# Kernel tuning notes

Hardware: AMD Instinct MI355X
Metric: run time of the kernel (lower is better)

The kernel has to match this reference:

```python
import jax, jax.numpy as jnp
import numpy as np

HEADS = 16
DIM_HEAD = 64
HEIGHT = 16
KERNEL = 5
DILATION = 1
ALPHA = 32 ** 2


def stable_softmax(t, axis=-1, alpha=ALPHA):
    t = t / alpha
    t = t - jax.lax.stop_gradient(jnp.max(t, axis=axis, keepdims=True))
    return jax.nn.softmax(t * alpha, axis=axis)


def setup_inputs() -> dict:
    key = jax.random.key(0)
    ks = jax.random.split(key, 5)
    b, n, dim = 4, 4097, 1024
    inner = HEADS * DIM_HEAD
    x = jax.random.normal(ks[0], (b, n, dim), dtype=jnp.float32)
    w_qkv = jax.random.normal(ks[1], (dim, 3 * inner), dtype=jnp.float32) * (dim ** -0.5)
    w_out = jax.random.normal(ks[2], (inner, dim), dtype=jnp.float32) * (inner ** -0.5)
    b_out = jax.random.normal(ks[3], (dim,), dtype=jnp.float32) * 0.02
    w_th = jax.random.normal(ks[4], (HEADS, HEADS), dtype=jnp.float32) * (HEADS ** -0.5)
    return {"x": x, "w_qkv": w_qkv, "w_out": w_out, "b_out": b_out, "w_th": w_th}


def reference(x, w_qkv, w_out, b_out, w_th):
    b, n, dim = x.shape
    h, d = HEADS, DIM_HEAD
    height, K, dil = HEIGHT, KERNEL, DILATION
    pad = dil * (K - 1) // 2
    scale = d ** -0.5
    kernel_numel = K * height

    # pad (n-1) non-BOS tokens to a multiple of height (static shapes)
    seq_pad = (-(n - 1)) % height
    xp = jnp.pad(x, ((0, 0), (0, seq_pad), (0, 0))) if seq_pad > 0 else x

    qkv = xp @ w_qkv  # [b, np, 3*inner]
    q, k, v = jnp.split(qkv, 3, axis=-1)

    if n == 1:  # bos-only path
        return v @ w_out + b_out

    out_bos = v[:, :1]  # [b, 1, inner]

    def to_heads(t):
        return t.reshape(b, -1, h, d).transpose(0, 2, 1, 3)  # [b,h,np,d]

    q, k, v = map(to_heads, (q, k, v))
    q = q * scale

    k_bos, k = k[:, :, 0], k[:, :, 1:]
    v_bos, v = v[:, :, 0], v[:, :, 1:]
    q = q[:, :, 1:]

    X = q.shape[2] // height  # number of timesteps

    # k, v as 2D grids [b,h,X,height,d]; unfold local windows along timestep axis
    k = k.reshape(b, h, X, height, d)
    v = v.reshape(b, h, X, height, d)
    kp = jnp.pad(k, ((0, 0), (0, 0), (pad, pad), (0, 0), (0, 0)))
    vp = jnp.pad(v, ((0, 0), (0, 0), (pad, pad), (0, 0), (0, 0)))
    idx = jnp.arange(X)[:, None] + jnp.arange(K)[None, :] * dil  # [X, K]
    kw = kp[:, :, idx].reshape(b, h, X, kernel_numel, d)  # [b,h,X,K*height,d]
    vw = vp[:, :, idx].reshape(b, h, X, kernel_numel, d)

    # prepend BOS key/value to every window
    kb = jnp.broadcast_to(k_bos[:, :, None, None, :], (b, h, X, 1, d))
    vb = jnp.broadcast_to(v_bos[:, :, None, None, :], (b, h, X, 1, d))
    kw = jnp.concatenate([kb, kw], axis=3)  # [b,h,X,1+kn,d]
    vw = jnp.concatenate([vb, vw], axis=3)

    qw = q.reshape(b, h, X, height, d)  # [b,h,X,height,d]
    sim = jnp.einsum('bhnid,bhnjd->bhnij', qw, kw)  # [b,h,X,height,1+kn]

    # causal mask over unfolded windows (BOS column never masked)
    seq_len = X * height
    q_range = jnp.arange(seq_len).reshape(X, height)
    k_range = jnp.pad(jnp.arange(seq_len).reshape(X, height), ((pad, pad), (0, 0)),
                      constant_values=seq_len)
    kr = k_range[idx].reshape(X, kernel_numel)  # [X, kn]
    mask = q_range[:, :, None] < kr[:, None, :]  # [X, height, kn]
    mask = jnp.pad(mask, ((0, 0), (0, 0), (1, 0)), constant_values=False)

    mask_value = -jnp.finfo(sim.dtype).max
    sim = jnp.where(mask[None, None], mask_value, sim)

    attn = stable_softmax(sim, axis=-1)
    # talking heads: 1x1x1 Conv3d over head channels == head mixing matmul
    attn = jnp.einsum('gh,bhnij->bgnij', w_th, attn)

    out = jnp.einsum('bhnij,bhnjd->bhnid', attn, vw)  # [b,h,X,height,d]
    out = out.transpose(0, 2, 3, 1, 4).reshape(b, X * height, h * d)
    out = jnp.concatenate([out_bos, out], axis=1)
    return (out @ w_out + b_out)[:, :n]
```

## Files before the change

kernel.cpp:

```cpp
#include <hip/hip_runtime.h>
#include <stdint.h>

typedef unsigned short u16;
typedef unsigned int u32;
typedef __attribute__((ext_vector_type(8))) short bf16x8;
typedef __attribute__((ext_vector_type(4))) float f32x4;

__device__ __forceinline__ float bf2f(u16 u) {
    union { u32 i; float f; } v; v.i = ((u32)u) << 16; return v.f;
}
__device__ __forceinline__ u16 f2bf(float f) {
    union { float f; u32 i; } v; v.f = f;
    u32 x = v.i;
    u32 r = (x + 0x7FFFu + ((x >> 16) & 1u)) >> 16;
    return (u16)r;
}

__device__ __forceinline__ void gld_lds16(const void* g, void* l) {
    __builtin_amdgcn_global_load_lds(
        (const __attribute__((address_space(1))) void*)g,
        (__attribute__((address_space(3))) void*)l, 16, 0, 0);
}

__global__ __launch_bounds__(256) void cvt_rows(
    const float* __restrict__ src, u16* __restrict__ dst, size_t total4) {
    size_t i = (size_t)blockIdx.x * 256 + threadIdx.x;
    if (i >= total4) return;
    const float4 v = ((const float4*)src)[i];
    u16 o[4] = {f2bf(v.x), f2bf(v.y), f2bf(v.z), f2bf(v.w)};
    *(unsigned long long*)(dst + i * 4) = *(unsigned long long*)o;
}

__global__ __launch_bounds__(256) void transpose_cvt(
    const float* __restrict__ src, u16* __restrict__ dst, int R, int C) {
    __shared__ float tile[32][33];
    int c0 = blockIdx.x * 32, r0 = blockIdx.y * 32;
    int tx = threadIdx.x & 31, ty = threadIdx.x >> 5;
    for (int rr = ty; rr < 32; rr += 8)
        tile[rr][tx] = src[(size_t)(r0 + rr) * C + c0 + tx];
    __syncthreads();
    for (int rr = ty; rr < 32; rr += 8)
        dst[(size_t)(c0 + rr) * R + r0 + tx] = f2bf(tile[tx][rr]);
}

template <int MODE>
__global__ __launch_bounds__(512) void gemm_bt2(
    const u16* __restrict__ A, const u16* __restrict__ Bt,
    const float* __restrict__ bias, void* __restrict__ Cv,
    int M, int N, int K) {
    __shared__ u16 lds[2][2][256 * 64];
    int tid = threadIdx.x;
    int wid = tid >> 6, lane = tid & 63;
    int lr = lane & 15, lq = lane >> 4;
    int wr = wid >> 2, wc = wid & 3;
    int m0 = blockIdx.x * 256, n0 = blockIdx.y * 256;
    int NT = K >> 6;

    f32x4 acc[8][4] = {};

    #define STAGE(t, buf)                                                     \
    do {                                                                      \
        int k0 = (t) << 6;                                                    \
        _Pragma("unroll")                                                     \
        for (int w = 0; w < 4; ++w) {                                         \
            int g = w * 512 + tid;                                            \
            int row = g >> 3;                                                 \
            int cdat = (g & 7) ^ ((row & 7) ^ ((row >> 3) & 1));              \
            int gm = m0 + row; if (gm >= M) gm = M - 1;                       \
            gld_lds16(A + (size_t)gm * K + k0 + cdat * 8,                     \
                      &lds[buf][0][g * 8]);                                   \
        }                                                                     \
        _Pragma("unroll")                                                     \
        for (int w = 0; w < 4; ++w) {                                         \
            int g = w * 512 + tid;                                            \
            int row = g >> 3;                                                 \
            int cdat = (g & 7) ^ ((row & 7) ^ ((row >> 3) & 1));              \
            int gn = n0 + row;                                                \
            gld_lds16(Bt + (size_t)gn * K + k0 + cdat * 8,                    \
                      &lds[buf][1][g * 8]);                                   \
        }                                                                     \
    } while (0)

    STAGE(0, 0);
    STAGE(1, 1);

    for (int t = 0; t < NT; ++t) {
        int buf = t & 1;
        if (t + 1 < NT) asm volatile("s_waitcnt vmcnt(8)" ::: "memory");
        else            asm volatile("s_waitcnt vmcnt(0)" ::: "memory");
        asm volatile("s_barrier" ::: "memory");
        const u16* Ab = &lds[buf][0][0];
        const u16* Bb = &lds[buf][1][0];
        #pragma unroll
        for (int ks = 0; ks < 2; ++ks) {
            int c = ks * 4 + lq;
            bf16x8 a[8], b[4];
            #pragma unroll
            for (int mi = 0; mi < 8; ++mi) {
                int r = wr * 128 + mi * 16 + lr;
                int cs = c ^ ((r & 7) ^ ((r >> 3) & 1));
                a[mi] = *(const bf16x8*)&Ab[r * 64 + cs * 8];
            }
            #pragma unroll
            for (int ni = 0; ni < 4; ++ni) {
                int r = wc * 64 + ni * 16 + lr;
                int cs = c ^ ((r & 7) ^ ((r >> 3) & 1));
                b[ni] = *(const bf16x8*)&Bb[r * 64 + cs * 8];
            }
            __builtin_amdgcn_s_setprio(1);
            #pragma unroll
            for (int mi = 0; mi < 8; ++mi)
                #pragma unroll
                for (int ni = 0; ni < 4; ++ni)
                    acc[mi][ni] = __builtin_amdgcn_mfma_f32_16x16x32_bf16(
                        a[mi], b[ni], acc[mi][ni], 0, 0, 0);
            __builtin_amdgcn_s_setprio(0);
        }
        asm volatile("s_barrier" ::: "memory");
        if (t + 2 < NT) STAGE(t + 2, buf);
    }
    #undef STAGE

    #pragma unroll
    for (int mi = 0; mi < 8; ++mi)
        #pragma unroll
        for (int ni = 0; ni < 4; ++ni) {
            int col = n0 + wc * 64 + ni * 16 + lr;
            float bv = (MODE == 1) ? bias[col] : 0.0f;
            #pragma unroll
            for (int r = 0; r < 4; ++r) {
                int row = m0 + wr * 128 + mi * 16 + lq * 4 + r;
                if (row < M) {
                    if (MODE == 0)
                        ((u16*)Cv)[(size_t)row * N + col] = f2bf(acc[mi][ni][r]);
                    else
                        ((float*)Cv)[(size_t)row * N + col] = acc[mi][ni][r] + bv;
                }
            }
        }
}

__global__ __launch_bounds__(256) void bos_copy(
    const u16* __restrict__ qkv, u16* __restrict__ attn_out) {
    int b = blockIdx.x;
    int c = blockIdx.y * 256 + threadIdx.x;
    attn_out[(size_t)b * 4097 * 1024 + c] =
        qkv[(size_t)b * 4097 * 3072 + 2048 + c];
}

__device__ __forceinline__ int pswz(int j, int i, int h) {
    int byte = j * 512 + i * 32 + h * 2;
    int sw = ((j & 7) ^ ((j >> 3) & 7) ^ ((i >> 2) & 3)) & 7;
    return byte ^ (sw << 4);
}

__global__ __launch_bounds__(256) void attn_kernel(
    const u16* __restrict__ qkv, const float* __restrict__ w_th,
    u16* __restrict__ attn_out) {
    __shared__ u16 P[64 * 16 * 16];
    __shared__ u16 vt[4][2048];
    __shared__ float wth_s[256];

    int tid = threadIdx.x;
    int wid = tid >> 6, lane = tid & 63;
    int x = blockIdx.x;
    int b = blockIdx.y;
    size_t base = (size_t)b * 4097 * 3072;
    int lr = lane & 15;
    int lq = lane >> 4;
    int lk8 = lq * 8;

    wth_s[tid] = w_th[tid];

    for (int hh = 0; hh < 4; ++hh) {
        int h = wid * 4 + hh;
        const u16* qp = qkv + base + (size_t)(1 + x * 16 + lr) * 3072 + h * 64;
        bf16x8 aq0 = *(const bf16x8*)(qp + lk8);
        bf16x8 aq1 = *(const bf16x8*)(qp + 32 + lk8);
        f32x4 acc[4];
        #pragma unroll
        for (int jt = 0; jt < 4; ++jt) {
            int j = jt * 16 + lr;
            int tpos = x * 16 - 32 + (j - 1);
            int t = (j > 0 && tpos >= 0 && tpos < 4096) ? tpos + 1 : 0;
            const u16* kp = qkv + base + (size_t)t * 3072 + 1024 + h * 64;
            bf16x8 bk0 = *(const bf16x8*)(kp + lk8);
            bf16x8 bk1 = *(const bf16x8*)(kp + 32 + lk8);
            f32x4 c = {};
            c = __builtin_amdgcn_mfma_f32_16x16x32_bf16(aq0, bk0, c, 0, 0, 0);
            c = __builtin_amdgcn_mfma_f32_16x16x32_bf16(aq1, bk1, c, 0, 0, 0);
            acc[jt] = c;
        }
        float m[4], s[4], p[4][4];
        #pragma unroll
        for (int r = 0; r < 4; ++r) m[r] = -3.0e38f;
        #pragma unroll
        for (int jt = 0; jt < 4; ++jt) {
            int j = jt * 16 + lr;
            int tpos = x * 16 - 32 + (j - 1);
            bool jvalid = (j == 0) || (tpos >= 0);
            #pragma unroll
            for (int r = 0; r < 4; ++r) {
                int i = lq * 4 + r;
                bool keep = jvalid && (j == 0 || j <= i + 33);
                float v = keep ? acc[jt][r] * 0.125f : -3.0e38f;
                p[jt][r] = v;
                m[r] = fmaxf(m[r], v);
            }
        }
        #pragma unroll
        for (int r = 0; r < 4; ++r) {
            float v = m[r];
            v = fmaxf(v, __shfl_xor(v, 1));
            v = fmaxf(v, __shfl_xor(v, 2));
            v = fmaxf(v, __shfl_xor(v, 4));
            v = fmaxf(v, __shfl_xor(v, 8));
            m[r] = v; s[r] = 0.0f;
        }
        #pragma unroll
        for (int jt = 0; jt < 4; ++jt)
            #pragma unroll
            for (int r = 0; r < 4; ++r) {
                float e = __expf(p[jt][r] - m[r]);
                p[jt][r] = e; s[r] += e;
            }
        #pragma unroll
        for (int r = 0; r < 4; ++r) {
            float v = s[r];
            v += __shfl_xor(v, 1); v += __shfl_xor(v, 2);
            v += __shfl_xor(v, 4); v += __shfl_xor(v, 8);
            s[r] = 1.0f / v;
        }
        #pragma unroll
        for (int jt = 0; jt < 4; ++jt) {
            int j = jt * 16 + lr;
            #pragma unroll
            for (int r = 0; r < 4; ++r) {
                int i = lq * 4 + r;
                *(u16*)((char*)P + pswz(j, i, h)) = f2bf(p[jt][r] * s[r]);
            }
        }
    }
    __syncthreads();

    const u16* vtw = &vt[wid][0];
    int jloc = lane >> 1, dh = lane & 1;
    for (int gg = 0; gg < 4; ++gg) {
        int g = wid * 4 + gg;
        float wth[16];
        #pragma unroll
        for (int h2 = 0; h2 < 16; ++h2) wth[h2] = wth_s[g * 16 + h2];
        f32x4 oacc[4] = {};
        #pragma unroll
        for (int kk = 0; kk < 2; ++kk) {
            {
                int jg = kk * 32 + jloc;
                int tpos = x * 16 - 32 + (jg - 1);
                int t = (jg > 0 && tpos >= 0 && tpos < 4096) ? tpos + 1 : 0;
                const u16* src = qkv + base + (size_t)t * 3072 + 2048 + g * 64
                               + dh * 8;
                #pragma unroll
                for (int w = 0; w < 4; ++w)
                    gld_lds16(src + w * 16, &vt[wid][w * 512 + lane * 8]);
            }
            bf16x8 av;
            #pragma unroll
            for (int e = 0; e < 8; ++e) {
                int j = kk * 32 + lk8 + e;
                bf16x8 v0 = *(const bf16x8*)((const char*)P + pswz(j, lr, 0));
                bf16x8 v1 = *(const bf16x8*)((const char*)P + pswz(j, lr, 8));
                float s0 = 0.0f, s1 = 0.0f;
                #pragma unroll
                for (int h2 = 0; h2 < 8; ++h2) {
                    s0 += wth[h2]     * bf2f((u16)v0[h2]);
                    s1 += wth[h2 + 8] * bf2f((u16)v1[h2]);
                }
                av[e] = (short)f2bf(s0 + s1);
            }
            asm volatile("s_waitcnt vmcnt(0)" ::: "memory");
            #pragma unroll
            for (int dt = 0; dt < 4; ++dt) {
                bf16x8 bv;
                #pragma unroll
                for (int e = 0; e < 8; ++e)
                    bv[e] = (short)vtw[dt * 512 + (lk8 + e) * 16 + lr];
                oacc[dt] = __builtin_amdgcn_mfma_f32_16x16x32_bf16(
                    av, bv, oacc[dt], 0, 0, 0);
            }
        }
        #pragma unroll
        for (int dt = 0; dt < 4; ++dt) {
            int col = g * 64 + dt * 16 + lr;
            #pragma unroll
            for (int r = 0; r < 4; ++r) {
                int i = lq * 4 + r;
                size_t row = (size_t)b * 4097 + 1 + (size_t)x * 16 + i;
                attn_out[row * 1024 + col] = f2bf(oacc[dt][r]);
            }
        }
    }
}

extern "C" void kernel_launch(void* const* d_in, const int* in_sizes, int n_in,
                              void* d_out, int out_size, void* d_ws, size_t ws_size,
                              hipStream_t stream) {
    const float* x     = (const float*)d_in[0];
    const float* w_qkv = (const float*)d_in[1];
    const float* w_out = (const float*)d_in[2];
    const float* b_out = (const float*)d_in[3];
    const float* w_th  = (const float*)d_in[4];
    float* out = (float*)d_out;

    const int M = 4 * 4097;
    u16* qkv      = (u16*)d_ws;
    u16* wqkvT    = qkv + (size_t)M * 3072;
    u16* woutT    = wqkvT + (size_t)3072 * 1024;
    u16* xb       = woutT + (size_t)1024 * 1024;
    u16* attn_out = xb;

    transpose_cvt<<<dim3(96, 32), 256, 0, stream>>>(w_qkv, wqkvT, 1024, 3072);
    transpose_cvt<<<dim3(32, 32), 256, 0, stream>>>(w_out, woutT, 1024, 1024);

    size_t total4 = (size_t)M * 1024 / 4;
    cvt_rows<<<(int)((total4 + 255) / 256), 256, 0, stream>>>(x, xb, total4);

    int mt = (M + 255) / 256;
    gemm_bt2<0><<<dim3(mt, 3072 / 256), 512, 0, stream>>>(
        xb, wqkvT, nullptr, qkv, M, 3072, 1024);

    bos_copy<<<dim3(4, 4), 256, 0, stream>>>(qkv, attn_out);
    attn_kernel<<<dim3(256, 4), 256, 0, stream>>>(qkv, w_th, attn_out);

    gemm_bt2<1><<<dim3(mt, 1024 / 256), 512, 0, stream>>>(
        attn_out, woutT, b_out, out, M, 1024, 1024);
}
```

Before: 305.8 us.

## Use 128x256 GEMM tiles with triple-buffered LDS and interleaved prefetch

The bf16 GEMM tile shrinks from 256x256 to 128x256, which halves the accumulator registers and doubles the grid size. LDS moves from double to triple buffering, and the global->LDS loads for step t+2 are spread across both k-substeps instead of being issued after the compute. This aims to raise occupancy and wave count on 256 CUs and to overlap loads with MFMA better. In exchange it adds more barriers per iteration and lowers arithmetic intensity per tile.

```diff
diff --git a/kernel.cpp b/kernel.cpp
--- a/kernel.cpp
+++ b/kernel.cpp
@@ -43,93 +43,106 @@
         dst[(size_t)(c0 + rr) * R + r0 + tx] = f2bf(tile[tx][rr]);
 }
 
+#define EROW(r) ((((r) & 7) ^ (((r) >> 3) & 1)))
 template <int MODE>
-__global__ __launch_bounds__(512) void gemm_bt2(
+__global__ __launch_bounds__(512) void gemm_bt3(
     const u16* __restrict__ A, const u16* __restrict__ Bt,
     const float* __restrict__ bias, void* __restrict__ Cv,
     int M, int N, int K) {
-    __shared__ u16 lds[2][2][256 * 64];
+    __shared__ u16 Asb[3][128 * 64];
+    __shared__ u16 Bsb[3][256 * 64];
     int tid = threadIdx.x;
     int wid = tid >> 6, lane = tid & 63;
     int lr = lane & 15, lq = lane >> 4;
     int wr = wid >> 2, wc = wid & 3;
-    int m0 = blockIdx.x * 256, n0 = blockIdx.y * 256;
+    int m0 = blockIdx.x * 128, n0 = blockIdx.y * 256;
     int NT = K >> 6;
-
-    f32x4 acc[8][4] = {};
-
-    #define STAGE(t, buf)                                                     \
-    do {                                                                      \
-        int k0 = (t) << 6;                                                    \
-        _Pragma("unroll")                                                     \
-        for (int w = 0; w < 4; ++w) {                                         \
-            int g = w * 512 + tid;                                            \
-            int row = g >> 3;                                                 \
-            int cdat = (g & 7) ^ ((row & 7) ^ ((row >> 3) & 1));              \
-            int gm = m0 + row; if (gm >= M) gm = M - 1;                       \
-            gld_lds16(A + (size_t)gm * K + k0 + cdat * 8,                     \
-                      &lds[buf][0][g * 8]);                                   \
-        }                                                                     \
-        _Pragma("unroll")                                                     \
-        for (int w = 0; w < 4; ++w) {                                         \
-            int g = w * 512 + tid;                                            \
-            int row = g >> 3;                                                 \
-            int cdat = (g & 7) ^ ((row & 7) ^ ((row >> 3) & 1));              \
-            int gn = n0 + row;                                                \
-            gld_lds16(Bt + (size_t)gn * K + k0 + cdat * 8,                    \
-                      &lds[buf][1][g * 8]);                                   \
-        }                                                                     \
+    f32x4 acc[4][4] = {};
+
+    #define STAGE_AU(u, t, bi)                                               \
+    do {                                                                     \
+        int g = (u) * 512 + tid;                                             \
+        int row = g >> 3;                                                    \
+        int c = (g & 7) ^ EROW(row);                                         \
+        int gm = m0 + row; if (gm >= M) gm = M - 1;                          \
+        gld_lds16(A + (size_t)gm * K + ((t) << 6) + c * 8,                   \
+                  &Asb[bi][g * 8]);                                          \
     } while (0)
-
-    STAGE(0, 0);
-    STAGE(1, 1);
-
+    #define STAGE_BU(u, t, bi)                                               \
+    do {                                                                     \
+        int g = (u) * 512 + tid;                                             \
+        int row = g >> 3;                                                    \
+        int c = (g & 7) ^ EROW(row);                                         \
+        gld_lds16(Bt + (size_t)(n0 + row) * K + ((t) << 6) + c * 8,          \
+                  &Bsb[bi][g * 8]);                                          \
+    } while (0)
+
+    STAGE_AU(0, 0, 0); STAGE_AU(1, 0, 0);
+    STAGE_BU(0, 0, 0); STAGE_BU(1, 0, 0); STAGE_BU(2, 0, 0); STAGE_BU(3, 0, 0);
+    STAGE_AU(0, 1, 1); STAGE_AU(1, 1, 1);
+    STAGE_BU(0, 1, 1); STAGE_BU(1, 1, 1); STAGE_BU(2, 1, 1); STAGE_BU(3, 1, 1);
+
+    int bcur = 0;
     for (int t = 0; t < NT; ++t) {
-        int buf = t & 1;
-        if (t + 1 < NT) asm volatile("s_waitcnt vmcnt(8)" ::: "memory");
+        if (t + 1 < NT) asm volatile("s_waitcnt vmcnt(6)" ::: "memory");
         else            asm volatile("s_waitcnt vmcnt(0)" ::: "memory");
         asm volatile("s_barrier" ::: "memory");
-        const u16* Ab = &lds[buf][0][0];
-        const u16* Bb = &lds[buf][1][0];
+        const u16* Ab = &Asb[bcur][0];
+        const u16* Bb = &Bsb[bcur][0];
+        int bst = bcur + 2; if (bst >= 3) bst -= 3;
+        bool st = (t + 2 < NT);
         #pragma unroll
         for (int ks = 0; ks < 2; ++ks) {
             int c = ks * 4 + lq;
-            bf16x8 a[8], b[4];
-            #pragma unroll
-            for (int mi = 0; mi < 8; ++mi) {
-                int r = wr * 128 + mi * 16 + lr;
-                int cs = c ^ ((r & 7) ^ ((r >> 3) & 1));
+            bf16x8 a[4], b[4];
+            #pragma unroll
+            for (int mi = 0; mi < 4; ++mi) {
+                int r = wr * 64 + mi * 16 + lr;
+                int cs = c ^ EROW(r);
                 a[mi] = *(const bf16x8*)&Ab[r * 64 + cs * 8];
             }
             #pragma unroll
             for (int ni = 0; ni < 4; ++ni) {
                 int r = wc * 64 + ni * 16 + lr;
-                int cs = c ^ ((r & 7) ^ ((r >> 3) & 1));
+                int cs = c ^ EROW(r);
                 b[ni] = *(const bf16x8*)&Bb[r * 64 + cs * 8];
             }
+            if (st) {
+                if (ks == 0) {
+                    STAGE_AU(0, t + 2, bst); STAGE_AU(1, t + 2, bst);
+                    STAGE_BU(0, t + 2, bst);
+                } else {
+                    STAGE_BU(1, t + 2, bst); STAGE_BU(2, t + 2, bst);
+                    STAGE_BU(3, t + 2, bst);
+                }
+            }
+            asm volatile("s_barrier" ::: "memory");
+            asm volatile("s_waitcnt lgkmcnt(0)" ::: "memory");
+            __builtin_amdgcn_sched_barrier(0);
             __builtin_amdgcn_s_setprio(1);
             #pragma unroll
-            for (int mi = 0; mi < 8; ++mi)
+            for (int mi = 0; mi < 4; ++mi)
                 #pragma unroll
                 for (int ni = 0; ni < 4; ++ni)
                     acc[mi][ni] = __builtin_amdgcn_mfma_f32_16x16x32_bf16(
                         a[mi], b[ni], acc[mi][ni], 0, 0, 0);
             __builtin_amdgcn_s_setprio(0);
-        }
-        asm volatile("s_barrier" ::: "memory");
-        if (t + 2 < NT) STAGE(t + 2, buf);
+            asm volatile("s_barrier" ::: "memory");
+        }
+        bcur = bcur + 1; if (bcur == 3) bcur = 0;
     }
-    #undef STAGE
+    #undef STAGE_AU
+    #undef STAGE_BU
 
     #pragma unroll
-    for (int mi = 0; mi < 8; ++mi)
+    for (int mi = 0; mi < 4; ++mi)
         #pragma unroll
         for (int ni = 0; ni < 4; ++ni) {
             int col = n0 + wc * 64 + ni * 16 + lr;
             float bv = (MODE == 1) ? bias[col] : 0.0f;
             #pragma unroll
             for (int r = 0; r < 4; ++r) {
-                int row = m0 + wr * 128 + mi * 16 + lq * 4 + r;
+                int row = m0 + wr * 64 + mi * 16 + lq * 4 + r;
                 if (row < M) {
                     if (MODE == 0)
                         ((u16*)Cv)[(size_t)row * N + col] = f2bf(acc[mi][ni][r]);
@@ -324,13 +337,13 @@
     size_t total4 = (size_t)M * 1024 / 4;
     cvt_rows<<<(int)((total4 + 255) / 256), 256, 0, stream>>>(x, xb, total4);
 
-    int mt = (M + 255) / 256;
-    gemm_bt2<0><<<dim3(mt, 3072 / 256), 512, 0, stream>>>(
+    int mt = (M + 127) / 128;
+    gemm_bt3<0><<<dim3(mt, 3072 / 256), 512, 0, stream>>>(
         xb, wqkvT, nullptr, qkv, M, 3072, 1024);
 
     bos_copy<<<dim3(4, 4), 256, 0, stream>>>(qkv, attn_out);
     attn_kernel<<<dim3(256, 4), 256, 0, stream>>>(qkv, w_th, attn_out);
 
-    gemm_bt2<1><<<dim3(mt, 1024 / 256), 512, 0, stream>>>(
+    gemm_bt3<1><<<dim3(mt, 1024 / 256), 512, 0, stream>>>(
         attn_out, woutT, b_out, out, M, 1024, 1024);
 }
```

Result: slower. 312.5 us (+2.2%).
